# Performance work log

Hardware: AMD Instinct MI355X
Metric: run time of the kernel (lower is better)

Reference implementation:

```python
import jax, jax.numpy as jnp
import numpy as np

EMBED_DIM = 128
HIDDEN_DIM = 32
BN_EPS = 1e-5


def setup_inputs() -> dict:
    key = jax.random.key(0)
    ks = jax.random.split(key, 11)
    B, N, D, H = 16, 2048, EMBED_DIM, HIDDEN_DIM
    s_d = 1.0 / np.sqrt(D)
    return {
        "f_in": jax.random.normal(ks[0], (B, N, D), dtype=jnp.float32),
        "w_q": jax.random.uniform(ks[1], (H, D), jnp.float32, -s_d, s_d),
        "b_q": jax.random.uniform(ks[2], (H,), jnp.float32, -s_d, s_d),
        "w_k": jax.random.uniform(ks[3], (H, D), jnp.float32, -s_d, s_d),
        "b_k": jax.random.uniform(ks[4], (H,), jnp.float32, -s_d, s_d),
        "w_v": jax.random.uniform(ks[5], (D, D), jnp.float32, -s_d, s_d),
        "b_v": jax.random.uniform(ks[6], (D,), jnp.float32, -s_d, s_d),
        "w_l": jax.random.uniform(ks[7], (D, D), jnp.float32, -s_d, s_d),
        "b_l": jax.random.uniform(ks[8], (D,), jnp.float32, -s_d, s_d),
        "bn_gamma": jnp.ones((D,), jnp.float32),
        "bn_beta": jnp.zeros((D,), jnp.float32),
    }


def reference(f_in, w_q, b_q, w_k, b_k, w_v, b_v, w_l, b_l, bn_gamma, bn_beta):
    # Q/K/V projections: (B, N, D) -> (B, N, h) / (B, N, D)
    q = jnp.einsum("bnd,hd->bnh", f_in, w_q) + b_q
    k = jnp.einsum("bnd,hd->bnh", f_in, w_k) + b_k
    v = jnp.einsum("bnd,ed->bne", f_in, w_v) + b_v
    # scores (B, N, N); softmax over dim=1 (query axis), then L1-renorm over keys
    a = jnp.einsum("bnh,bmh->bnm", q, k)
    a = jax.nn.softmax(a, axis=1)
    a = a / jnp.sum(a, axis=2, keepdims=True)
    f_sa = jnp.einsum("bnm,bme->bne", a, v)
    # LBR: Linear -> BatchNorm (training stats over B and N) -> ReLU, residual add
    x = f_in - f_sa
    y = jnp.einsum("bnd,ed->bne", x, w_l) + b_l
    mean = jnp.mean(y, axis=(0, 1))
    var = jnp.var(y, axis=(0, 1))  # biased, as BatchNorm uses for normalization
    y = bn_gamma * (y - mean) * jax.lax.rsqrt(var + BN_EPS) + bn_beta
    return jax.nn.relu(y) + f_sa
```

## Files before the change

kernel.cpp:

```cpp
#include <hip/hip_runtime.h>
#include <stdint.h>

#define NB 16
#define NN 2048
#define ND 128
#define NH 32
#define NS (NB*NN)

typedef __attribute__((ext_vector_type(8))) short bf16x8;
typedef __attribute__((ext_vector_type(4))) float f32x4;
typedef __attribute__((ext_vector_type(16))) float f32x16;
typedef __attribute__((ext_vector_type(2))) int i32x2;

__device__ __forceinline__ unsigned short f2bf(float f){
  union { float f; unsigned int u; } v; v.f = f;
  unsigned int r = v.u + 0x7fffu + ((v.u >> 16) & 1u);
  return (unsigned short)(r >> 16);
}
__device__ __forceinline__ float bf2f(unsigned short u){
  union { unsigned int u; float f; } v; v.u = ((unsigned int)u) << 16;
  return v.f;
}
__device__ __forceinline__ float fexp2(float x){
  float r; asm("v_exp_f32 %0, %1" : "=v"(r) : "v"(x)); return r;
}
__device__ __forceinline__ void pswap(unsigned int &x, unsigned int &y){
#if __has_builtin(__builtin_amdgcn_permlane32_swap)
  i32x2 r = __builtin_amdgcn_permlane32_swap((int)x, (int)y, false, false);
  x = (unsigned int)r[0]; y = (unsigned int)r[1];
#else
  unsigned int sx = (unsigned int)__shfl_xor((int)x, 32, 64);
  unsigned int sy = (unsigned int)__shfl_xor((int)y, 32, 64);
  bool hi = ((threadIdx.x & 63) >> 5) != 0;
  unsigned int nx = hi ? sy : x;
  unsigned int ny = hi ? y  : sx;
  x = nx; y = ny;
#endif
}

__global__ __launch_bounds__(256) void k_prep(const float* wq, const float* wk, const float* wv, const float* wl,
                                              unsigned short* oq, unsigned short* ok, unsigned short* ov, unsigned short* ol){
  int i = blockIdx.x*256 + threadIdx.x;
  if (i < 4096) oq[i] = f2bf(wq[i]);
  else if (i < 8192) ok[i-4096] = f2bf(wk[i-4096]);
  else if (i < 24576) ov[i-8192] = f2bf(wv[i-8192]);
  else if (i < 40960) ol[i-24576] = f2bf(wl[i-24576]);
}

__global__ __launch_bounds__(256) void k_qkv(const float* f, const unsigned short* wbq, const unsigned short* wbk,
                                             const unsigned short* wbv, const float* bq, const float* bk, const float* bv,
                                             unsigned short* Qb, unsigned short* Kb, unsigned short* Vb){
  int tid = threadIdx.x, wave = tid>>6, lane = tid&63, lr = lane&15, lg = lane>>4;
  long r0 = (long)blockIdx.x*64 + wave*16;
  bf16x8 a[4];
  const float* frow = f + (r0 + lr)*ND;
  #pragma unroll
  for (int ks=0; ks<4; ks++){
    const float* p = frow + ks*32 + lg*8;
    bf16x8 t;
    #pragma unroll
    for (int j=0;j<8;j++) t[j] = (short)f2bf(p[j]);
    a[ks] = t;
  }
  #pragma unroll
  for (int cs=0; cs<12; cs++){
    const unsigned short* wsrc; const float* bsrc; int cl;
    if (cs<2){ wsrc=wbq; bsrc=bq; cl=cs*16; }
    else if (cs<4){ wsrc=wbk; bsrc=bk; cl=(cs-2)*16; }
    else { wsrc=wbv; bsrc=bv; cl=(cs-4)*16; }
    f32x4 acc = {0.f,0.f,0.f,0.f};
    #pragma unroll
    for (int ks=0;ks<4;ks++){
      bf16x8 b = *(const bf16x8*)(wsrc + (cl+lr)*ND + ks*32 + lg*8);
      acc = __builtin_amdgcn_mfma_f32_16x16x32_bf16(a[ks], b, acc, 0, 0, 0);
    }
    float bias = bsrc[cl + lr];
    #pragma unroll
    for (int r=0;r<4;r++){
      float v = acc[r] + bias;
      if (cs<2) v *= 1.4426950408889634f;
      long row = r0 + lg*4 + r;
      if (cs<2) Qb[row*NH + cl+lr] = f2bf(v);
      else if (cs<4) Kb[row*NH + cl+lr] = f2bf(v);
      else Vb[row*ND + cl+lr] = f2bf(v);
    }
  }
}

__global__ __launch_bounds__(256) void k_csv(const unsigned short* Qb, const unsigned short* Kb,
                                             const unsigned short* Vb, unsigned short* VT){
  __shared__ unsigned short tr[128][65];
  __shared__ float wsh[64];
  int tid=threadIdx.x, wave=tid>>6, lane=tid&63, lr=lane&15, lg=lane>>4;
  int wg = (blockIdx.x & 7)*64 + (blockIdx.x >> 3);
  int b = wg >> 5;
  int m0 = (wg & 31)*64;
  const unsigned short* Qbb = Qb + (long)b*NN*NH;
  const unsigned short* Kbb = Kb + (long)b*NN*NH;
  const unsigned short* Vbb = Vb + ((long)b*NN + m0)*ND;
  bf16x8 vreg[4];
  #pragma unroll
  for (int it=0; it<4; it++){
    int i = it*256 + tid;
    int r = i >> 4, c8 = (i & 15)*8;
    vreg[it] = *(const bf16x8*)(Vbb + r*ND + c8);
  }
  bf16x8 kf = *(const bf16x8*)(Kbb + (m0 + wave*16 + lr)*NH + lg*8);
  float csum = 0.f;
  for (int n0=0; n0<NN; n0+=64){
    #pragma unroll
    for (int u=0; u<4; u++){
      bf16x8 qf = *(const bf16x8*)(Qbb + (n0+u*16+lr)*NH + lg*8);
      f32x4 c = {0.f,0.f,0.f,0.f};
      c = __builtin_amdgcn_mfma_f32_16x16x32_bf16(qf, kf, c, 0, 0, 0);
      csum += fexp2(c[0]) + fexp2(c[1]) + fexp2(c[2]) + fexp2(c[3]);
    }
  }
  csum += __shfl_xor(csum, 16, 64);
  csum += __shfl_xor(csum, 32, 64);
  #pragma unroll
  for (int it=0; it<4; it++){
    int i = it*256 + tid;
    int r = i >> 4, c8 = (i & 15)*8;
    #pragma unroll
    for (int j=0;j<8;j++) tr[c8+j][r] = (unsigned short)vreg[it][j];
  }
  if (lg == 0) wsh[wave*16 + lr] = 1.f / csum;
  __syncthreads();
  unsigned short* VTb = VT + (long)b*160*NN;
  #pragma unroll
  for (int it=0; it<9; it++){
    int i = it*256 + tid;
    int e = i >> 4, m4 = (i & 15)*4;
    ushort4 o;
    if (e < 128){
      o.x = f2bf(bf2f(tr[e][m4+0]) * wsh[m4+0]);
      o.y = f2bf(bf2f(tr[e][m4+1]) * wsh[m4+1]);
      o.z = f2bf(bf2f(tr[e][m4+2]) * wsh[m4+2]);
      o.w = f2bf(bf2f(tr[e][m4+3]) * wsh[m4+3]);
    } else if (e == 128){
      o.x = f2bf(wsh[m4+0]); o.y = f2bf(wsh[m4+1]);
      o.z = f2bf(wsh[m4+2]); o.w = f2bf(wsh[m4+3]);
    } else { o.x = o.y = o.z = o.w = 0; }
    *(ushort4*)(VTb + (long)e*NN + m0 + m4) = o;
  }
  {
    int e = 144 + (tid >> 4), m4 = (tid & 15)*4;
    ushort4 z; z.x = z.y = z.z = z.w = 0;
    *(ushort4*)(VTb + (long)e*NN + m0 + m4) = z;
  }
}

__global__ __launch_bounds__(256) void k_pv(const unsigned short* Qb, const unsigned short* Kb,
                                            const unsigned short* VT, unsigned short* pnum, float* pden){
  __shared__ __align__(16) unsigned char vts[3][20480];
  int tid=threadIdx.x, wave=tid>>6, lane=tid&63;
  int l31 = lane & 31, H = lane >> 5;
  int wg = (blockIdx.x & 7)*64 + (blockIdx.x >> 3);
  int half = wg & 1;
  int bq = wg >> 1;
  int b = bq >> 4;
  int q0 = (bq & 15)*128 + wave*32;
  int mbase = half*1024;
  const int NT2 = 16;
  const unsigned short* Qbb = Qb + (long)b*NN*NH;
  const unsigned short* Kbb = Kb + (long)b*NN*NH;
  const unsigned short* VTb = VT + (long)b*160*NN;

  auto stageV = [&](int buf, int m0c){
    #pragma unroll
    for (int t=0;t<5;t++){
      int i = wave*5 + t;
      int e = i*8 + (lane>>3);
      int sblk = (lane&7) ^ (e&7);
      __builtin_amdgcn_global_load_lds(
        (const __attribute__((address_space(1))) unsigned int*)(VTb + (long)e*NN + m0c + sblk*8),
        (__attribute__((address_space(3))) unsigned int*)(&vts[buf][i*1024]), 16, 0, 0);
    }
  };

  bf16x8 qf0 = *(const bf16x8*)(Qbb + (long)(q0 + l31)*NH + 8*H);
  bf16x8 qf1 = *(const bf16x8*)(Qbb + (long)(q0 + l31)*NH + 16 + 8*H);

  f32x16 acc[5];
  #pragma unroll
  for (int c=0;c<5;c++)
    #pragma unroll
    for (int r=0;r<16;r++) acc[c][r] = 0.f;

  union U { unsigned int u[4]; bf16x8 v; };

  auto SCORE = [&](bf16x8 a0, bf16x8 a1, bf16x8 b0, bf16x8 b1, unsigned int* w){
    #pragma unroll
    for (int t=0;t<2;t++){
      f32x16 s;
      #pragma unroll
      for (int r=0;r<16;r++) s[r] = 0.f;
      s = __builtin_amdgcn_mfma_f32_32x32x16_bf16(t ? b0 : a0, qf0, s, 0, 0, 0);
      s = __builtin_amdgcn_mfma_f32_32x32x16_bf16(t ? b1 : a1, qf1, s, 0, 0, 0);
      #pragma unroll
      for (int r=0;r<16;r++) s[r] = fexp2(s[r]);
      unsigned int pk[8];
      #pragma unroll
      for (int p=0;p<8;p++)
        asm("v_cvt_pk_bf16_f32 %0, %1, %2" : "=v"(pk[p]) : "v"(s[2*p]), "v"(s[2*p+1]));
      pswap(pk[0], pk[2]);
      pswap(pk[1], pk[3]);
      pswap(pk[4], pk[6]);
      pswap(pk[5], pk[7]);
      #pragma unroll
      for (int j=0;j<8;j++) w[t*8+j] = pk[j];
    }
  };

  auto PV = [&](const unsigned int* w, const unsigned char* vcur){
    __builtin_amdgcn_s_setprio(1);
    #pragma unroll
    for (int t=0;t<2;t++){
      #pragma unroll
      for (int ksl=0; ksl<2; ksl++){
        int KS = 2*t + ksl;
        U fa;
        #pragma unroll
        for (int i2=0;i2<4;i2++) fa.u[i2] = w[t*8 + ksl*4 + i2];
        #pragma unroll
        for (int c=0;c<5;c++){
          int e = c*32 + l31;
          bf16x8 vb = *(const bf16x8*)(vcur + (e<<7) + (((2*KS + H) ^ (e&7))<<4));
          acc[c] = __builtin_amdgcn_mfma_f32_32x32x16_bf16(fa.v, vb, acc[c], 0, 0, 0);
        }
      }
    }
    __builtin_amdgcn_s_setprio(0);
  };

  stageV(0, mbase);
  stageV(1, mbase + 64);
  asm volatile("" ::: "memory");
  bf16x8 k00 = *(const bf16x8*)(Kbb + (long)(mbase + l31)*NH + 8*H);
  bf16x8 k01 = *(const bf16x8*)(Kbb + (long)(mbase + l31)*NH + 16 + 8*H);
  bf16x8 k10 = *(const bf16x8*)(Kbb + (long)(mbase + 32 + l31)*NH + 8*H);
  bf16x8 k11 = *(const bf16x8*)(Kbb + (long)(mbase + 32 + l31)*NH + 16 + 8*H);
  asm volatile("s_waitcnt vmcnt(0)" ::: "memory");
  unsigned int eA[16], eB[16];
  SCORE(k00, k01, k10, k11, eA);

  int vc = 0, vs = 2;
  auto BODY = [&](int it, unsigned int* Ein, unsigned int* Eout){
    __builtin_amdgcn_s_barrier();
    asm volatile("" ::: "memory");
    bool pf = (it + 1 < NT2);
    bf16x8 n00, n01, n10, n11;
    if (pf){
      long mb = mbase + (long)(it+1)*64;
      n00 = *(const bf16x8*)(Kbb + (mb + l31)*NH + 8*H);
      n01 = *(const bf16x8*)(Kbb + (mb + l31)*NH + 16 + 8*H);
      n10 = *(const bf16x8*)(Kbb + (mb + 32 + l31)*NH + 8*H);
      n11 = *(const bf16x8*)(Kbb + (mb + 32 + l31)*NH + 16 + 8*H);
    }
    asm volatile("" ::: "memory");
    if (it + 2 < NT2) stageV(vs, mbase + (it+2)*64);
    asm volatile("" ::: "memory");
    PV(Ein, &vts[vc][0]);
    if (pf){
      if (it + 2 < NT2) asm volatile("s_waitcnt vmcnt(5)" ::: "memory");
      else              asm volatile("s_waitcnt vmcnt(0)" ::: "memory");
      __builtin_amdgcn_sched_barrier(0);
      SCORE(n00, n01, n10, n11, Eout);
    }
    vc = (vc==2)?0:vc+1;
    vs = (vs==2)?0:vs+1;
  };

  for (int it2 = 0; it2 < NT2; it2 += 2){
    BODY(it2,   eA, eB);
    BODY(it2+1, eB, eA);
  }

  unsigned short* pn = pnum + (long)half*NS*ND + (long)b*NN*ND;
  float* pd = pden + (long)half*NS + (long)b*NN;
  #pragma unroll
  for (int r=0;r<16;r++){
    int rho = (r&3) + 8*(r>>2) + 4*H;
    long q = q0 + rho;
    #pragma unroll
    for (int c=0;c<4;c++)
      pn[q*ND + c*32 + l31] = f2bf(acc[c][r]);
    if (l31 == 0) pd[q] = acc[4][r];
  }
}

__global__ __launch_bounds__(256) void k_lin(const float* f, const unsigned short* pnum, const float* pden,
                                             const unsigned short* wbl, const float* bl,
                                             unsigned short* fsab, unsigned short* ybuf, float* part){
  __shared__ float psum[4][128], psq[4][128];
  int tid=threadIdx.x, wave=tid>>6, lane=tid&63, lr=lane&15, lg=lane>>4;
  long r0 = (long)blockIdx.x*64 + wave*16;
  long row = r0 + lr;
  float rinv = 1.f / (pden[row] + pden[NS + row]);
  bf16x8 a[4];
  {
    const float* fr = f + row*ND;
    const unsigned short* p0 = pnum + row*ND;
    const unsigned short* p1 = pnum + (long)NS*ND + row*ND;
    #pragma unroll
    for (int ks=0;ks<4;ks++){
      bf16x8 v0 = *(const bf16x8*)(p0 + ks*32 + lg*8);
      bf16x8 v1 = *(const bf16x8*)(p1 + ks*32 + lg*8);
      bf16x8 t, fs;
      #pragma unroll
      for (int j=0;j<8;j++){
        int d = ks*32 + lg*8 + j;
        float sa = (bf2f((unsigned short)v0[j]) + bf2f((unsigned short)v1[j])) * rinv;
        fs[j] = (short)f2bf(sa);
        t[j] = (short)f2bf(fr[d] - bf2f((unsigned short)fs[j]));
      }
      a[ks] = t;
      *(bf16x8*)(fsab + row*ND + ks*32 + lg*8) = fs;
    }
  }
  #pragma unroll
  for (int cs=0;cs<8;cs++){
    f32x4 acc = {0.f,0.f,0.f,0.f};
    #pragma unroll
    for (int ks=0;ks<4;ks++){
      bf16x8 bfr = *(const bf16x8*)(wbl + (cs*16+lr)*ND + ks*32 + lg*8);
      acc = __builtin_amdgcn_mfma_f32_16x16x32_bf16(a[ks], bfr, acc, 0, 0, 0);
    }
    float bias = bl[cs*16+lr];
    float l1=0.f, l2=0.f;
    #pragma unroll
    for (int r=0;r<4;r++){
      float y = acc[r] + bias;
      ybuf[(r0 + lg*4 + r)*ND + cs*16 + lr] = f2bf(y);
      l1 += y; l2 += y*y;
    }
    l1 += __shfl_xor(l1,16,64); l1 += __shfl_xor(l1,32,64);
    l2 += __shfl_xor(l2,16,64); l2 += __shfl_xor(l2,32,64);
    if (lg==0){ psum[wave][cs*16+lr] = l1; psq[wave][cs*16+lr] = l2; }
  }
  __syncthreads();
  if (tid < 128){
    float t1 = psum[0][tid]+psum[1][tid]+psum[2][tid]+psum[3][tid];
    float t2 = psq[0][tid]+psq[1][tid]+psq[2][tid]+psq[3][tid];
    part[tid*512 + blockIdx.x] = t1;
    part[65536 + tid*512 + blockIdx.x] = t2;
  }
}

__global__ __launch_bounds__(64) void k_bnred(const float* part, const float* gamma, const float* beta, float* bnstat){
  int c = blockIdx.x, t = threadIdx.x;
  float s=0.f, q=0.f;
  for (int i=t; i<512; i+=64){ s += part[c*512+i]; q += part[65536 + c*512+i]; }
  #pragma unroll
  for (int m=1; m<64; m<<=1){ s += __shfl_xor(s,m,64); q += __shfl_xor(q,m,64); }
  if (t==0){
    float mean = s * (1.f/(float)NS);
    float var  = q * (1.f/(float)NS) - mean*mean;
    float rstd = rsqrtf(var + 1e-5f);
    float sc = gamma[c]*rstd;
    bnstat[c] = sc;
    bnstat[128+c] = beta[c] - mean*sc;
  }
}

__global__ __launch_bounds__(256) void k_final(const unsigned short* ybuf, const unsigned short* fsab, const float* bnstat,
                                               float* out){
  long i0 = ((long)blockIdx.x*256 + threadIdx.x)*8;
  int c0 = (int)(i0 & (ND-1));
  bf16x8 yv = *(const bf16x8*)(ybuf + i0);
  bf16x8 fv = *(const bf16x8*)(fsab + i0);
  f32x4 o0, o1;
  #pragma unroll
  for (int j=0;j<8;j++){
    int c = c0 + j;
    float v = bf2f((unsigned short)yv[j]) * bnstat[c] + bnstat[128+c];
    v = v > 0.f ? v : 0.f;
    float r = v + bf2f((unsigned short)fv[j]);
    if (j<4) o0[j] = r; else o1[j-4] = r;
  }
  *(f32x4*)(out + i0) = o0;
  *(f32x4*)(out + i0 + 4) = o1;
}

extern "C" void kernel_launch(void* const* d_in, const int* in_sizes, int n_in,
                              void* d_out, int out_size, void* d_ws, size_t ws_size,
                              hipStream_t stream){
  const float* f_in  = (const float*)d_in[0];
  const float* w_q   = (const float*)d_in[1];
  const float* b_q   = (const float*)d_in[2];
  const float* w_k   = (const float*)d_in[3];
  const float* b_k   = (const float*)d_in[4];
  const float* w_v   = (const float*)d_in[5];
  const float* b_v   = (const float*)d_in[6];
  const float* w_l   = (const float*)d_in[7];
  const float* b_l   = (const float*)d_in[8];
  const float* gamma = (const float*)d_in[9];
  const float* beta  = (const float*)d_in[10];
  float* out = (float*)d_out;
  char* ws = (char*)d_ws;

  unsigned short* wbq = (unsigned short*)(ws + 0);
  unsigned short* wbk = (unsigned short*)(ws + 8192);
  unsigned short* wbv = (unsigned short*)(ws + 16384);
  unsigned short* wbl = (unsigned short*)(ws + 49152);
  unsigned short* Qb  = (unsigned short*)(ws + 81920);
  float*          part= (float*)(ws + 81920);
  unsigned short* Kb  = (unsigned short*)(ws + 2179072);
  unsigned short* VT  = (unsigned short*)(ws + 4276224);
  unsigned short* ybuf= (unsigned short*)(ws + 4276224);
  unsigned short* Vb  = (unsigned short*)(ws + 14761984);
  unsigned short* fsab= (unsigned short*)(ws + 14761984);
  unsigned short* pnum= (unsigned short*)(ws + 23150592);
  float*          pden= (float*)(ws + 39927808);
  float*          bnst= (float*)(ws + 40189952);

  k_prep  <<<160, 256, 0, stream>>>(w_q, w_k, w_v, w_l, wbq, wbk, wbv, wbl);
  k_qkv   <<<512, 256, 0, stream>>>(f_in, wbq, wbk, wbv, b_q, b_k, b_v, Qb, Kb, Vb);
  k_csv   <<<512, 256, 0, stream>>>(Qb, Kb, Vb, VT);
  k_pv    <<<512, 256, 0, stream>>>(Qb, Kb, VT, pnum, pden);
  k_lin   <<<512, 256, 0, stream>>>(f_in, pnum, pden, wbl, b_l, fsab, ybuf, part);
  k_bnred <<<128, 64, 0, stream>>>(part, gamma, beta, bnst);
  k_final <<<2048,256, 0, stream>>>(ybuf, fsab, bnst, out);
}
```

Baseline: 114.7 us.

## Fuse linear, BatchNorm reduction and final epilogue into one cooperative kernel

Replaces the k_lin, k_bnred and k_final kernels with a single cooperative kernel that keeps the linear outputs in registers and f_sa in swizzled shared memory. Two grid-wide syncs separate the partial-statistics pass, the per-channel reduction done by the first 128 blocks, and the normalize/ReLU/residual epilogue. This removes the ybuf and fsab round trips through global memory and two kernel launches. It also vectorizes the f_in loads into float4 in k_qkv and the tail kernel. In exchange it requires all 512 blocks to be co-resident, adds grid-sync cost, and writes the output with scalar strided stores.

```diff
diff --git a/kernel.cpp b/kernel.cpp
--- a/kernel.cpp
+++ b/kernel.cpp
@@ -1,5 +1,8 @@
 #include <hip/hip_runtime.h>
+#include <hip/hip_cooperative_groups.h>
 #include <stdint.h>
+
+namespace cg = cooperative_groups;
 
 #define NB 16
 #define NN 2048
@@ -53,13 +56,14 @@
   int tid = threadIdx.x, wave = tid>>6, lane = tid&63, lr = lane&15, lg = lane>>4;
   long r0 = (long)blockIdx.x*64 + wave*16;
   bf16x8 a[4];
-  const float* frow = f + (r0 + lr)*ND;
+  const float4* frow4 = (const float4*)(f + (r0 + lr)*ND);
   #pragma unroll
   for (int ks=0; ks<4; ks++){
-    const float* p = frow + ks*32 + lg*8;
+    int base = ks*8 + lg*2;
+    float4 x0 = frow4[base], x1 = frow4[base+1];
     bf16x8 t;
-    #pragma unroll
-    for (int j=0;j<8;j++) t[j] = (short)f2bf(p[j]);
+    t[0]=(short)f2bf(x0.x); t[1]=(short)f2bf(x0.y); t[2]=(short)f2bf(x0.z); t[3]=(short)f2bf(x0.w);
+    t[4]=(short)f2bf(x1.x); t[5]=(short)f2bf(x1.y); t[6]=(short)f2bf(x1.z); t[7]=(short)f2bf(x1.w);
     a[ks] = t;
   }
   #pragma unroll
@@ -290,35 +294,41 @@
   }
 }
 
-__global__ __launch_bounds__(256) void k_lin(const float* f, const unsigned short* pnum, const float* pden,
-                                             const unsigned short* wbl, const float* bl,
-                                             unsigned short* fsab, unsigned short* ybuf, float* part){
+__global__ __launch_bounds__(256, 2) void k_tail(const float* f, const unsigned short* pnum, const float* pden,
+                                                 const unsigned short* wbl, const float* bl,
+                                                 const float* gamma, const float* beta,
+                                                 float* part, float* bnst, float* out){
+  __shared__ unsigned short fsl[64][128];
   __shared__ float psum[4][128], psq[4][128];
+  cg::grid_group grid = cg::this_grid();
   int tid=threadIdx.x, wave=tid>>6, lane=tid&63, lr=lane&15, lg=lane>>4;
   long r0 = (long)blockIdx.x*64 + wave*16;
   long row = r0 + lr;
   float rinv = 1.f / (pden[row] + pden[NS + row]);
   bf16x8 a[4];
   {
-    const float* fr = f + row*ND;
+    const float4* fr4 = (const float4*)(f + row*ND);
     const unsigned short* p0 = pnum + row*ND;
     const unsigned short* p1 = pnum + (long)NS*ND + row*ND;
     #pragma unroll
     for (int ks=0;ks<4;ks++){
-      bf16x8 v0 = *(const bf16x8*)(p0 + ks*32 + lg*8);
-      bf16x8 v1 = *(const bf16x8*)(p1 + ks*32 + lg*8);
+      int c8 = ks*4 + lg;
+      float4 x0 = fr4[c8*2], x1 = fr4[c8*2+1];
+      bf16x8 v0 = *(const bf16x8*)(p0 + c8*8);
+      bf16x8 v1 = *(const bf16x8*)(p1 + c8*8);
+      float xf[8] = {x0.x,x0.y,x0.z,x0.w,x1.x,x1.y,x1.z,x1.w};
       bf16x8 t, fs;
       #pragma unroll
       for (int j=0;j<8;j++){
-        int d = ks*32 + lg*8 + j;
         float sa = (bf2f((unsigned short)v0[j]) + bf2f((unsigned short)v1[j])) * rinv;
         fs[j] = (short)f2bf(sa);
-        t[j] = (short)f2bf(fr[d] - bf2f((unsigned short)fs[j]));
+        t[j] = (short)f2bf(xf[j] - bf2f((unsigned short)fs[j]));
       }
       a[ks] = t;
-      *(bf16x8*)(fsab + row*ND + ks*32 + lg*8) = fs;
-    }
-  }
+      *(bf16x8*)(&fsl[wave*16 + lr][(c8 ^ (lr&7))*8]) = fs;
+    }
+  }
+  float yv[8][4];
   #pragma unroll
   for (int cs=0;cs<8;cs++){
     f32x4 acc = {0.f,0.f,0.f,0.f};
@@ -332,7 +342,7 @@
     #pragma unroll
     for (int r=0;r<4;r++){
       float y = acc[r] + bias;
-      ybuf[(r0 + lg*4 + r)*ND + cs*16 + lr] = f2bf(y);
+      yv[cs][r] = y;
       l1 += y; l2 += y*y;
     }
     l1 += __shfl_xor(l1,16,64); l1 += __shfl_xor(l1,32,64);
@@ -346,41 +356,41 @@
     part[tid*512 + blockIdx.x] = t1;
     part[65536 + tid*512 + blockIdx.x] = t2;
   }
-}
-
-__global__ __launch_bounds__(64) void k_bnred(const float* part, const float* gamma, const float* beta, float* bnstat){
-  int c = blockIdx.x, t = threadIdx.x;
-  float s=0.f, q=0.f;
-  for (int i=t; i<512; i+=64){ s += part[c*512+i]; q += part[65536 + c*512+i]; }
-  #pragma unroll
-  for (int m=1; m<64; m<<=1){ s += __shfl_xor(s,m,64); q += __shfl_xor(q,m,64); }
-  if (t==0){
-    float mean = s * (1.f/(float)NS);
-    float var  = q * (1.f/(float)NS) - mean*mean;
-    float rstd = rsqrtf(var + 1e-5f);
-    float sc = gamma[c]*rstd;
-    bnstat[c] = sc;
-    bnstat[128+c] = beta[c] - mean*sc;
-  }
-}
-
-__global__ __launch_bounds__(256) void k_final(const unsigned short* ybuf, const unsigned short* fsab, const float* bnstat,
-                                               float* out){
-  long i0 = ((long)blockIdx.x*256 + threadIdx.x)*8;
-  int c0 = (int)(i0 & (ND-1));
-  bf16x8 yv = *(const bf16x8*)(ybuf + i0);
-  bf16x8 fv = *(const bf16x8*)(fsab + i0);
-  f32x4 o0, o1;
-  #pragma unroll
-  for (int j=0;j<8;j++){
-    int c = c0 + j;
-    float v = bf2f((unsigned short)yv[j]) * bnstat[c] + bnstat[128+c];
-    v = v > 0.f ? v : 0.f;
-    float r = v + bf2f((unsigned short)fv[j]);
-    if (j<4) o0[j] = r; else o1[j-4] = r;
-  }
-  *(f32x4*)(out + i0) = o0;
-  *(f32x4*)(out + i0 + 4) = o1;
+  grid.sync();
+  if (blockIdx.x < 128){
+    int c = blockIdx.x;
+    float s=0.f, q=0.f;
+    for (int i=tid; i<512; i+=256){ s += part[c*512+i]; q += part[65536 + c*512+i]; }
+    #pragma unroll
+    for (int m=1; m<64; m<<=1){ s += __shfl_xor(s,m,64); q += __shfl_xor(q,m,64); }
+    if (lane==0){ psum[0][wave] = s; psq[0][wave] = q; }
+    __syncthreads();
+    if (tid==0){
+      float S  = psum[0][0]+psum[0][1]+psum[0][2]+psum[0][3];
+      float Q2 = psq[0][0]+psq[0][1]+psq[0][2]+psq[0][3];
+      float mean = S * (1.f/(float)NS);
+      float var  = Q2 * (1.f/(float)NS) - mean*mean;
+      float rstd = rsqrtf(var + 1e-5f);
+      float sc = gamma[c]*rstd;
+      bnst[c] = sc;
+      bnst[128+c] = beta[c] - mean*sc;
+    }
+  }
+  grid.sync();
+  #pragma unroll
+  for (int cs=0;cs<8;cs++){
+    int c = cs*16 + lr;
+    float sc = bnst[c], sh = bnst[128+c];
+    int c8 = c >> 3, off = c & 7;
+    #pragma unroll
+    for (int r=0;r<4;r++){
+      int rl = wave*16 + lg*4 + r;
+      unsigned short fsv = fsl[rl][((c8 ^ (rl&7))*8) + off];
+      float v = yv[cs][r]*sc + sh;
+      v = v > 0.f ? v : 0.f;
+      out[(r0 + lg*4 + r)*ND + c] = v + bf2f(fsv);
+    }
+  }
 }
 
 extern "C" void kernel_launch(void* const* d_in, const int* in_sizes, int n_in,
@@ -408,9 +418,7 @@
   float*          part= (float*)(ws + 81920);
   unsigned short* Kb  = (unsigned short*)(ws + 2179072);
   unsigned short* VT  = (unsigned short*)(ws + 4276224);
-  unsigned short* ybuf= (unsigned short*)(ws + 4276224);
   unsigned short* Vb  = (unsigned short*)(ws + 14761984);
-  unsigned short* fsab= (unsigned short*)(ws + 14761984);
   unsigned short* pnum= (unsigned short*)(ws + 23150592);
   float*          pden= (float*)(ws + 39927808);
   float*          bnst= (float*)(ws + 40189952);
@@ -419,7 +427,8 @@
   k_qkv   <<<512, 256, 0, stream>>>(f_in, wbq, wbk, wbv, b_q, b_k, b_v, Qb, Kb, Vb);
   k_csv   <<<512, 256, 0, stream>>>(Qb, Kb, Vb, VT);
   k_pv    <<<512, 256, 0, stream>>>(Qb, Kb, VT, pnum, pden);
-  k_lin   <<<512, 256, 0, stream>>>(f_in, pnum, pden, wbl, b_l, fsab, ybuf, part);
-  k_bnred <<<128, 64, 0, stream>>>(part, gamma, beta, bnst);
-  k_final <<<2048,256, 0, stream>>>(ybuf, fsab, bnst, out);
-}
+
+  void* kargs[] = {(void*)&f_in, (void*)&pnum, (void*)&pden, (void*)&wbl, (void*)&b_l,
+                   (void*)&gamma, (void*)&beta, (void*)&part, (void*)&bnst, (void*)&out};
+  hipLaunchCooperativeKernel((void*)k_tail, dim3(512), dim3(256), kargs, 0, stream);
+}
```

Measured after the change: 238.3 us. +107.8%, slower.

## Stage Q tiles into LDS with async triple-buffered loads; vectorize f_in reads

Applied to the files above, without the earlier changes.

In the column-sum kernel, Q tiles are now brought into a swizzled shared-memory triple buffer with global_load_lds and consumed after waitcnt/barrier, so loads for later tiles overlap with MFMA and exp work instead of each wave issuing direct global reads in the loop. The qkv and linear kernels read f_in as float4 pairs rather than scalar floats, to get wider global loads. The pipeline adds per-iteration barriers and extra LDS use, which may lower occupancy.

```diff
diff --git a/kernel.cpp b/kernel.cpp
--- a/kernel.cpp
+++ b/kernel.cpp
@@ -53,13 +53,14 @@
   int tid = threadIdx.x, wave = tid>>6, lane = tid&63, lr = lane&15, lg = lane>>4;
   long r0 = (long)blockIdx.x*64 + wave*16;
   bf16x8 a[4];
-  const float* frow = f + (r0 + lr)*ND;
+  const float4* frow4 = (const float4*)(f + (r0 + lr)*ND);
   #pragma unroll
   for (int ks=0; ks<4; ks++){
-    const float* p = frow + ks*32 + lg*8;
+    int base = ks*8 + lg*2;
+    float4 x0 = frow4[base], x1 = frow4[base+1];
     bf16x8 t;
-    #pragma unroll
-    for (int j=0;j<8;j++) t[j] = (short)f2bf(p[j]);
+    t[0]=(short)f2bf(x0.x); t[1]=(short)f2bf(x0.y); t[2]=(short)f2bf(x0.z); t[3]=(short)f2bf(x0.w);
+    t[4]=(short)f2bf(x1.x); t[5]=(short)f2bf(x1.y); t[6]=(short)f2bf(x1.z); t[7]=(short)f2bf(x1.w);
     a[ks] = t;
   }
   #pragma unroll
@@ -91,6 +92,7 @@
                                              const unsigned short* Vb, unsigned short* VT){
   __shared__ unsigned short tr[128][65];
   __shared__ float wsh[64];
+  __shared__ __align__(16) unsigned char qs[3][4096];
   int tid=threadIdx.x, wave=tid>>6, lane=tid&63, lr=lane&15, lg=lane>>4;
   int wg = (blockIdx.x & 7)*64 + (blockIdx.x >> 3);
   int b = wg >> 5;
@@ -98,6 +100,16 @@
   const unsigned short* Qbb = Qb + (long)b*NN*NH;
   const unsigned short* Kbb = Kb + (long)b*NN*NH;
   const unsigned short* Vbb = Vb + ((long)b*NN + m0)*ND;
+
+  auto stageQ = [&](int buf, int n0){
+    int row = wave*16 + (lane>>2);
+    int blk = lane & 3;
+    int scol = (blk ^ ((row>>1)&3))*8;
+    __builtin_amdgcn_global_load_lds(
+      (const __attribute__((address_space(1))) unsigned int*)(Qbb + (long)(n0+row)*NH + scol),
+      (__attribute__((address_space(3))) unsigned int*)(&qs[buf][wave*1024]), 16, 0, 0);
+  };
+
   bf16x8 vreg[4];
   #pragma unroll
   for (int it=0; it<4; it++){
@@ -106,15 +118,28 @@
     vreg[it] = *(const bf16x8*)(Vbb + r*ND + c8);
   }
   bf16x8 kf = *(const bf16x8*)(Kbb + (m0 + wave*16 + lr)*NH + lg*8);
+  stageQ(0, 0);
+  stageQ(1, 64);
+
   float csum = 0.f;
-  for (int n0=0; n0<NN; n0+=64){
+  int qrd = (lg ^ ((lr>>1)&3)) << 4;
+  int qc = 0, qsn = 2;
+  for (int it = 0; it < 32; ++it){
+    if (it < 31) asm volatile("s_waitcnt vmcnt(1)" ::: "memory");
+    else         asm volatile("s_waitcnt vmcnt(0)" ::: "memory");
+    __builtin_amdgcn_s_barrier();
+    if (it + 2 < 32) stageQ(qsn, (it+2)*64);
+    asm volatile("" ::: "memory");
     #pragma unroll
     for (int u=0; u<4; u++){
-      bf16x8 qf = *(const bf16x8*)(Qbb + (n0+u*16+lr)*NH + lg*8);
+      int r = u*16 + lr;
+      bf16x8 qf = *(const bf16x8*)(&qs[qc][r*64 + qrd]);
       f32x4 c = {0.f,0.f,0.f,0.f};
       c = __builtin_amdgcn_mfma_f32_16x16x32_bf16(qf, kf, c, 0, 0, 0);
       csum += fexp2(c[0]) + fexp2(c[1]) + fexp2(c[2]) + fexp2(c[3]);
     }
+    qc = (qc==2)?0:qc+1;
+    qsn = (qsn==2)?0:qsn+1;
   }
   csum += __shfl_xor(csum, 16, 64);
   csum += __shfl_xor(csum, 32, 64);
@@ -300,23 +325,25 @@
   float rinv = 1.f / (pden[row] + pden[NS + row]);
   bf16x8 a[4];
   {
-    const float* fr = f + row*ND;
+    const float4* fr4 = (const float4*)(f + row*ND);
     const unsigned short* p0 = pnum + row*ND;
     const unsigned short* p1 = pnum + (long)NS*ND + row*ND;
     #pragma unroll
     for (int ks=0;ks<4;ks++){
-      bf16x8 v0 = *(const bf16x8*)(p0 + ks*32 + lg*8);
-      bf16x8 v1 = *(const bf16x8*)(p1 + ks*32 + lg*8);
+      int c8 = ks*4 + lg;
+      float4 x0 = fr4[c8*2], x1 = fr4[c8*2+1];
+      bf16x8 v0 = *(const bf16x8*)(p0 + c8*8);
+      bf16x8 v1 = *(const bf16x8*)(p1 + c8*8);
+      float xf[8] = {x0.x,x0.y,x0.z,x0.w,x1.x,x1.y,x1.z,x1.w};
       bf16x8 t, fs;
       #pragma unroll
       for (int j=0;j<8;j++){
-        int d = ks*32 + lg*8 + j;
         float sa = (bf2f((unsigned short)v0[j]) + bf2f((unsigned short)v1[j])) * rinv;
         fs[j] = (short)f2bf(sa);
-        t[j] = (short)f2bf(fr[d] - bf2f((unsigned short)fs[j]));
+        t[j] = (short)f2bf(xf[j] - bf2f((unsigned short)fs[j]));
       }
       a[ks] = t;
-      *(bf16x8*)(fsab + row*ND + ks*32 + lg*8) = fs;
+      *(bf16x8*)(fsab + row*ND + c8*8) = fs;
     }
   }
   #pragma unroll
```

Result: faster. 109.9 us (-4.2%).
